# Optimization experiments

Measured on AMD Instinct MI355X. Metric: run time of the kernel, lower is better.

The kernel has to match this reference:

```python
import jax, jax.numpy as jnp
import numpy as np

FRAMESIZE = 80


def setup_inputs() -> dict:
    key = jax.random.key(0)
    k1, k2 = jax.random.split(key)
    B, t, nbands = 32, 4000, 257
    H = jax.random.normal(k1, (B, t, nbands), dtype=jnp.float32)
    noise_u = jax.random.uniform(k2, (B, t, FRAMESIZE), dtype=jnp.float32)
    return {"H": H, "noise_u": noise_u}


def reference(H, noise_u):
    """Time-varying filtered noise via linear-phase LTV-FIR + overlap-add.

    H       : [B, t, nbands] half spectrum (real) of zero-phase filter
    noise_u : [B, t, framesize] uniform noise in [0, 1)
    returns : [B, t*framesize]
    """
    framesize = FRAMESIZE
    B, t, nbands = H.shape
    N = 2 * nbands - 1  # FIR length L (odd)

    # torch.hann_window default is periodic: w[n] = 0.5*(1 - cos(2*pi*n/N))
    hann = (0.5 * (1.0 - jnp.cos(2.0 * jnp.pi * jnp.arange(N) / N))).astype(jnp.float32)

    # zero-phase impulse response -> linear phase via circular shift, then window
    zero_phase = jnp.fft.irfft(H, n=N, axis=-1)              # [B, t, N]
    lin_phase = jnp.roll(zero_phase, nbands - 1, axis=-1)    # [B, t, N]
    firwin = lin_phase * hann                                # [B, t, N]
    L = N

    noise = noise_u * 2.0 - 1.0                              # uniform in [-1, 1)

    # full linear convolution per (B, t) frame via FFT (fftconvolve, mode='full')
    nfft = framesize + L - 1
    Fn = jnp.fft.rfft(noise, n=nfft, axis=-1)
    Ff = jnp.fft.rfft(firwin, n=nfft, axis=-1)
    filtered = jnp.fft.irfft(Fn * Ff, n=nfft, axis=-1)       # [B, t, framesize+L-1]

    # overlap-add with hop = framesize (the conv_transpose1d(eye) trick, done as
    # a direct strided scatter-add), then trim the L-1 tail as in the original
    out_len = t * framesize + L - 1
    idx = (jnp.arange(t)[:, None] * framesize + jnp.arange(nfft)[None, :]).reshape(-1)
    out = jnp.zeros((B, out_len), dtype=filtered.dtype)
    out = out.at[:, idx].add(filtered.reshape(B, -1))
    return out[:, : t * framesize]
```

## Files before the change

kernel.cpp:

```cpp
#include <hip/hip_runtime.h>
#include <stdint.h>

typedef unsigned short u16;
typedef unsigned int   u32;
typedef _Float16 f16;
typedef __attribute__((ext_vector_type(2))) _Float16 half2v;
typedef __attribute__((ext_vector_type(8))) _Float16 half8;
typedef __attribute__((ext_vector_type(4))) float f32x4;

#define TPB 320
#define FPB 25
#define NB 257
#define LF 513
#define FS 80
#define NCH 9
#define MT_TOTAL 33
#define HROW16 296
#define GROW 336
#define NROW 44
#define CONVT 314
#define TAB_ELEMS (MT_TOTAL*NCH*64*8)

__device__ __forceinline__ u32 pk2(float a, float b){
  return __builtin_bit_cast(u32, __builtin_amdgcn_cvt_pkrtz(a, b));
}
__device__ __forceinline__ float dot2(u32 a, u32 b, float c){
#if __has_builtin(__builtin_amdgcn_fdot2)
  return __builtin_amdgcn_fdot2(__builtin_bit_cast(half2v, a), __builtin_bit_cast(half2v, b), c, false);
#else
  half2v x = __builtin_bit_cast(half2v, a), y = __builtin_bit_cast(half2v, b);
  return fmaf((float)x[1], (float)y[1], fmaf((float)x[0], (float)y[0], c));
#endif
}

__global__ void build_table(u16* __restrict__ tab){
  int id = blockIdx.x * blockDim.x + threadIdx.x;
  if (id >= TAB_ELEMS) return;
  int j    = id & 7;
  int lane = (id >> 3) & 63;
  int cc   = (id >> 9) % NCH;
  int mt   = (id >> 9) / NCH;
  int tap  = mt * 16 + (lane & 15);
  int kslot= cc * 32 + (lane >> 4) * 8 + j;
  float val = 0.f;
  if (tap < LF){
    float hann = 0.5f - 0.5f * cosf(6.28318530717958647f * (float)tap / 513.f);
    if (kslot == 0){
      val = hann * (1.f / 513.f);
    } else if (kslot <= 256){
      int rr = (kslot * (tap + 257)) % 513;
      val = (2.f / 513.f) * hann * cosf((float)rr * (6.28318530717958647f / 513.f));
    }
  }
  f16 h = (f16)val;
  tab[id] = __builtin_bit_cast(u16, h);
}

__launch_bounds__(TPB, 5)
__global__ void fused(const float* __restrict__ Hg, const float* __restrict__ noiseg,
                      const u16* __restrict__ tab, float* __restrict__ out){
  __shared__ __align__(16) u32 Gu[FPB * GROW];
  __shared__ __align__(16) u32 Nu[FPB * NROW];

  const int tid  = threadIdx.x;
  const int lane = tid & 63;
  const int w    = tid >> 6;
  const int ln15 = lane & 15;
  const int q    = lane >> 4;
  const int blk  = blockIdx.x;
  const int f0   = blk * FPB;

  u16* Hlds = (u16*)Gu;

  #pragma unroll
  for (int e = 0; e < 12; ++e){
    int id = tid + TPB * e;
    if (id < FPB * 144){
      int r = id / 144, p = id % 144;
      const float* gp = Hg + (size_t)(f0 + r) * NB;
      u32 v = 0u;
      if (p < 128)       v = pk2(gp[2*p], gp[2*p+1]);
      else if (p == 128) v = pk2(gp[256], 0.f);
      *(u32*)&Hlds[r * HROW16 + 2 * p] = v;
    }
  }
  #pragma unroll
  for (int e = 0; e < 4; ++e){
    int id = tid + TPB * e;
    if (id < FPB * 40){
      int r = id / 40, m = id % 40;
      const float* np = noiseg + (size_t)(f0 + r) * FS + 2 * m;
      Nu[r * NROW + m] = pk2(np[0] * 2.f - 1.f, np[1] * 2.f - 1.f);
    }
  }
  if (tid < FPB){
    float n0 = noiseg[(size_t)(f0 + tid) * FS] * 2.f - 1.f;
    Nu[tid * NROW + 40] = 0u;
    Nu[tid * NROW + 41] = pk2(0.f, n0);
    Nu[tid * NROW + 42] = 0u;
    Nu[tid * NROW + 43] = 0u;
  }
  __syncthreads();

  const int base = (w < 3) ? 7 * w : 21 + 6 * (w - 3);
  const int cnt  = (w < 3) ? 7 : 6;
  f32x4 acc[7][2];
  #pragma unroll
  for (int a = 0; a < 7; ++a){ acc[a][0] = (f32x4){0,0,0,0}; acc[a][1] = (f32x4){0,0,0,0}; }
  const half8* tab8 = (const half8*)tab;
  for (int c = 0; c < NCH; ++c){
    half8 bfrag[2];
    #pragma unroll
    for (int nt = 0; nt < 2; ++nt)
      bfrag[nt] = *(const half8*)&Hlds[(nt*16 + ln15) * HROW16 + c*32 + q*8];
    #pragma unroll
    for (int mm = 0; mm < 7; ++mm){
      if (mm < cnt){
        half8 afrag = tab8[((base + mm) * NCH + c) * 64 + lane];
        #pragma unroll
        for (int nt = 0; nt < 2; ++nt)
          acc[mm][nt] = __builtin_amdgcn_mfma_f32_16x16x32_f16(afrag, bfrag[nt], acc[mm][nt], 0, 0, 0);
      }
    }
  }
  __syncthreads();

  #pragma unroll
  for (int mm = 0; mm < 7; ++mm){
    if (mm < cnt){
      int t0 = (base + mm)*16 + q*4;
      #pragma unroll
      for (int nt = 0; nt < 2; ++nt){
        int frame = nt*16 + ln15;
        if (frame < FPB){
          f32x4 v = acc[mm][nt];
          uint2 pk;
          pk.x = pk2(v.w, v.z);
          pk.y = pk2(v.y, v.x);
          *(uint2*)&Gu[frame * GROW + (294 - (t0 >> 1))] = pk;
        }
      }
    }
  }
  #pragma unroll
  for (int e = 0; e < 6; ++e){
    int id = tid + TPB * e;
    if (id < FPB * 72){
      int r = id / 72, s2 = id % 72;
      Gu[r * GROW + (s2 < 32 ? s2 : 264 + s2)] = 0u;
    }
  }
  __syncthreads();

  const bool lastB = (blk % 160) == 159;
  if (tid < CONVT && !(lastB && tid >= FPB * 10)){
    const int s8   = tid % 10;
    const int fTop = tid / 10;
    const int dMax = (s8 <= 3) ? 7 : 6;
    float ac[8];
    #pragma unroll
    for (int r = 0; r < 8; ++r) ac[r] = 0.f;

    #pragma unroll 1
    for (int d = 0; d <= 7; ++d){
      const int frel = fTop - d;
      if (d <= dMax && frel >= 0 && frel < FPB){
        const u32* Gr = Gu + frel * GROW;
        const u32* Nr = Nu + frel * NROW;
        const int V = 296 - 4*s8 - 40*d;
        u32 WA[44];
        #pragma unroll
        for (int qq = 0; qq < 11; ++qq){
          uint4 gq = *(const uint4*)(Gr + V - 4 + 4*qq);
          WA[4*qq]   = gq.x; WA[4*qq+1] = gq.y;
          WA[4*qq+2] = gq.z; WA[4*qq+3] = gq.w;
        }
        const u32 n0hi = Nr[41];
        uint4 naNext = *(const uint4*)(Nr);
        #pragma unroll
        for (int k = 0; k < 4; ++k)
          ac[2*k] = dot2(n0hi, WA[3-k], ac[2*k]);
        #pragma unroll
        for (int c = 0; c < 10; ++c){
          uint4 naCur = naNext;
          naNext = *(const uint4*)(Nr + 4*c + 4);
          u32 nAv[5] = {naCur.x, naCur.y, naCur.z, naCur.w, naNext.x};
          #pragma unroll
          for (int i = 0; i < 4; ++i){
            u32 a   = nAv[i];
            u32 sft = __builtin_amdgcn_alignbit(nAv[i+1], nAv[i], 16);
            #pragma unroll
            for (int k = 0; k < 4; ++k){
              ac[2*k]   = dot2(sft, WA[4*c+4+i-k], ac[2*k]);
              ac[2*k+1] = dot2(a,   WA[4*c+3+i-k], ac[2*k+1]);
            }
          }
        }
      }
    }
    const size_t s0 = (size_t)blk * (FPB*FS) + (size_t)tid * 8;
    if (tid >= 64 && tid < FPB * 10){
      *(float4*)&out[s0]     = make_float4(ac[0], ac[1], ac[2], ac[3]);
      *(float4*)&out[s0 + 4] = make_float4(ac[4], ac[5], ac[6], ac[7]);
    } else {
      #pragma unroll
      for (int r = 0; r < 8; ++r) atomicAdd(&out[s0 + r], ac[r]);
    }
  }
}

extern "C" void kernel_launch(void* const* d_in, const int* in_sizes, int n_in,
                              void* d_out, int out_size, void* d_ws, size_t ws_size,
                              hipStream_t stream){
  const float* Hg     = (const float*)d_in[0];
  const float* noiseg = (const float*)d_in[1];
  float* out = (float*)d_out;
  u16* tab = (u16*)d_ws;

  hipMemsetAsync(d_out, 0, (size_t)out_size * sizeof(float), stream);
  build_table<<<TAB_ELEMS / 256, 256, 0, stream>>>(tab);
  fused<<<(32 * 4000) / FPB, TPB, 0, stream>>>(Hg, noiseg, tab, out);
}
```

Measured before the change: 508.3 us.

## Shrink blocks to 16 frames with one MFMA N-tile and remap block order

Reduces frames per block from 25 to 16 so the GEMM uses a single 16-wide N tile with no wasted padded columns, and cuts the thread count to 256 with a higher launch-bound occupancy target. The accumulator array shrinks, lowering register pressure, and the G row stride is padded to 340. Block indices are interleaved across eight batch-chunks, which changes the order in which blocks are scheduled. The cost is more blocks, and therefore more boundary-overlap atomics and repeated per-block setup relative to useful work.

```diff
diff --git a/kernel.cpp b/kernel.cpp
--- a/kernel.cpp
+++ b/kernel.cpp
@@ -8,17 +8,18 @@
 typedef __attribute__((ext_vector_type(8))) _Float16 half8;
 typedef __attribute__((ext_vector_type(4))) float f32x4;
 
-#define TPB 320
-#define FPB 25
+#define TPB 256
+#define FPB 16
 #define NB 257
 #define LF 513
 #define FS 80
 #define NCH 9
 #define MT_TOTAL 33
 #define HROW16 296
-#define GROW 336
+#define GROW 340
 #define NROW 44
-#define CONVT 314
+#define CONVT 224
+#define BPB 250
 #define TAB_ELEMS (MT_TOTAL*NCH*64*8)
 
 __device__ __forceinline__ u32 pk2(float a, float b){
@@ -56,7 +57,7 @@
   tab[id] = __builtin_bit_cast(u16, h);
 }
 
-__launch_bounds__(TPB, 5)
+__launch_bounds__(TPB, 6)
 __global__ void fused(const float* __restrict__ Hg, const float* __restrict__ noiseg,
                       const u16* __restrict__ tab, float* __restrict__ out){
   __shared__ __align__(16) u32 Gu[FPB * GROW];
@@ -67,25 +68,23 @@
   const int w    = tid >> 6;
   const int ln15 = lane & 15;
   const int q    = lane >> 4;
-  const int blk  = blockIdx.x;
+  const int blk  = (int)(blockIdx.x % 8) * 1000 + (int)(blockIdx.x / 8);
   const int f0   = blk * FPB;
 
   u16* Hlds = (u16*)Gu;
 
   #pragma unroll
-  for (int e = 0; e < 12; ++e){
+  for (int e = 0; e < 9; ++e){
     int id = tid + TPB * e;
-    if (id < FPB * 144){
-      int r = id / 144, p = id % 144;
-      const float* gp = Hg + (size_t)(f0 + r) * NB;
-      u32 v = 0u;
-      if (p < 128)       v = pk2(gp[2*p], gp[2*p+1]);
-      else if (p == 128) v = pk2(gp[256], 0.f);
-      *(u32*)&Hlds[r * HROW16 + 2 * p] = v;
-    }
-  }
-  #pragma unroll
-  for (int e = 0; e < 4; ++e){
+    int r = id / 144, p = id % 144;
+    const float* gp = Hg + (size_t)(f0 + r) * NB;
+    u32 v = 0u;
+    if (p < 128)       v = pk2(gp[2*p], gp[2*p+1]);
+    else if (p == 128) v = pk2(gp[256], 0.f);
+    *(u32*)&Hlds[r * HROW16 + 2 * p] = v;
+  }
+  #pragma unroll
+  for (int e = 0; e < 3; ++e){
     int id = tid + TPB * e;
     if (id < FPB * 40){
       int r = id / 40, m = id % 40;
@@ -102,57 +101,46 @@
   }
   __syncthreads();
 
-  const int base = (w < 3) ? 7 * w : 21 + 6 * (w - 3);
-  const int cnt  = (w < 3) ? 7 : 6;
-  f32x4 acc[7][2];
-  #pragma unroll
-  for (int a = 0; a < 7; ++a){ acc[a][0] = (f32x4){0,0,0,0}; acc[a][1] = (f32x4){0,0,0,0}; }
+  const int base = (w == 0) ? 0 : (9 + 8 * (w - 1));
+  const int cnt  = (w == 0) ? 9 : 8;
+  f32x4 acc[9];
+  #pragma unroll
+  for (int a = 0; a < 9; ++a) acc[a] = (f32x4){0,0,0,0};
   const half8* tab8 = (const half8*)tab;
   for (int c = 0; c < NCH; ++c){
-    half8 bfrag[2];
+    half8 bfrag = *(const half8*)&Hlds[ln15 * HROW16 + c*32 + q*8];
     #pragma unroll
-    for (int nt = 0; nt < 2; ++nt)
-      bfrag[nt] = *(const half8*)&Hlds[(nt*16 + ln15) * HROW16 + c*32 + q*8];
-    #pragma unroll
-    for (int mm = 0; mm < 7; ++mm){
+    for (int mm = 0; mm < 9; ++mm){
       if (mm < cnt){
         half8 afrag = tab8[((base + mm) * NCH + c) * 64 + lane];
-        #pragma unroll
-        for (int nt = 0; nt < 2; ++nt)
-          acc[mm][nt] = __builtin_amdgcn_mfma_f32_16x16x32_f16(afrag, bfrag[nt], acc[mm][nt], 0, 0, 0);
+        acc[mm] = __builtin_amdgcn_mfma_f32_16x16x32_f16(afrag, bfrag, acc[mm], 0, 0, 0);
       }
     }
   }
   __syncthreads();
 
   #pragma unroll
-  for (int mm = 0; mm < 7; ++mm){
+  for (int mm = 0; mm < 9; ++mm){
     if (mm < cnt){
       int t0 = (base + mm)*16 + q*4;
-      #pragma unroll
-      for (int nt = 0; nt < 2; ++nt){
-        int frame = nt*16 + ln15;
-        if (frame < FPB){
-          f32x4 v = acc[mm][nt];
-          uint2 pk;
-          pk.x = pk2(v.w, v.z);
-          pk.y = pk2(v.y, v.x);
-          *(uint2*)&Gu[frame * GROW + (294 - (t0 >> 1))] = pk;
-        }
-      }
-    }
-  }
-  #pragma unroll
-  for (int e = 0; e < 6; ++e){
+      f32x4 v = acc[mm];
+      uint2 pk;
+      pk.x = pk2(v.w, v.z);
+      pk.y = pk2(v.y, v.x);
+      *(uint2*)&Gu[ln15 * GROW + (294 - (t0 >> 1))] = pk;
+    }
+  }
+  #pragma unroll
+  for (int e = 0; e < 5; ++e){
     int id = tid + TPB * e;
-    if (id < FPB * 72){
-      int r = id / 72, s2 = id % 72;
+    if (id < FPB * 76){
+      int r = id / 76, s2 = id % 76;
       Gu[r * GROW + (s2 < 32 ? s2 : 264 + s2)] = 0u;
     }
   }
   __syncthreads();
 
-  const bool lastB = (blk % 160) == 159;
+  const bool lastB = (blk % BPB) == (BPB - 1);
   if (tid < CONVT && !(lastB && tid >= FPB * 10)){
     const int s8   = tid % 10;
     const int fTop = tid / 10;
```

Result: slower. 532.9 us (+4.8%).
